# Kernel optimization log

Hardware: AMD Instinct MI355X
Metric: run time of the kernel (lower is better)

## Reference

```python
import jax, jax.numpy as jnp
import numpy as np
from jax import lax

# Model / data dims (match init_kwargs / input_specs)
B, SEQ_LEN, IN_DIM, HID, TGT, PRED_LEN = 64, 1024, 128, 256, 128, 192
NUM_SCALES, TOP_K, KS = 2, 3, 3
DN = ('NCHW', 'OIHW', 'NCHW')


def avg_pool1d(x):
    # stride-2 average pool over last axis: [B,C,T] -> [B,C,T//2]
    b, c, t = x.shape
    return x[..., : (t // 2) * 2].reshape(b, c, t // 2, 2).mean(-1)


def dsconv2d(z, dw_w, dw_b, pw_w, pw_b):
    # depthwise 3x3 (groups=C_in, SAME pad) + pointwise 1x1 (C_in -> HID)
    c = z.shape[1]
    y = lax.conv_general_dilated(z, dw_w, (1, 1), 'SAME',
                                 feature_group_count=c, dimension_numbers=DN)
    y = y + dw_b[None, :, None, None]
    y = lax.conv_general_dilated(y, pw_w, (1, 1), 'SAME', dimension_numbers=DN)
    return y + pw_b[None, :, None, None]


def mean_amplitudes(xm):
    # xm: [B,C,T]; mean |rfft| over batch and channels, DC component zeroed
    a = jnp.abs(jnp.fft.rfft(xm, axis=-1)).mean(axis=(0, 1))
    return a.at[0].set(0.0)


def topk_freqs(xm, k):
    # concrete (eager) top-k frequency indices -> python ints (mirrors .item())
    amps = mean_amplitudes(xm)
    idx = np.asarray(lax.top_k(amps, k)[1])
    return [max(1, int(i)) for i in idx]


def setup_inputs() -> dict:
    key = jax.random.key(0)
    ks = jax.random.split(key, 8)
    s = 0.05
    return {
        'x': jax.random.normal(ks[0], (B, SEQ_LEN, IN_DIM), jnp.float32),
        'dw_w': jax.random.normal(ks[1], (IN_DIM, 1, KS, KS), jnp.float32) * s,
        'dw_b': jnp.zeros((IN_DIM,), jnp.float32),
        'pw_w': jax.random.normal(ks[2], (HID, IN_DIM, 1, 1), jnp.float32) * s,
        'pw_b': jnp.zeros((HID,), jnp.float32),
        'w_t0': jax.random.normal(ks[3], (PRED_LEN, SEQ_LEN), jnp.float32) * s,
        'b_t0': jnp.zeros((PRED_LEN,), jnp.float32),
        'w_t1': jax.random.normal(ks[4], (PRED_LEN, SEQ_LEN // 2), jnp.float32) * s,
        'b_t1': jnp.zeros((PRED_LEN,), jnp.float32),
        'w_t2': jax.random.normal(ks[5], (PRED_LEN, SEQ_LEN // 4), jnp.float32) * s,
        'b_t2': jnp.zeros((PRED_LEN,), jnp.float32),
        'w_ch': jax.random.normal(ks[6], (TGT, HID), jnp.float32) * s,
        'b_ch': jnp.zeros((TGT,), jnp.float32),
        'scale_logits': jnp.zeros((NUM_SCALES + 1,), jnp.float32),
    }


def _forward(x, dw_w, dw_b, pw_w, pw_b, time_ws, time_bs, w_ch, b_ch,
             scale_logits, freqs_per_scale):
    x_ct = jnp.transpose(x, (0, 2, 1))  # [B,C,T]
    scales = [x_ct]
    for _ in range(NUM_SCALES):
        scales.append(avg_pool1d(scales[-1]))
    sw = jax.nn.softmax(scale_logits) * float(NUM_SCALES + 1)
    y_sum = 0.0
    for m, xm in enumerate(scales):
        t = xm.shape[-1]
        amps = mean_amplitudes(xm)
        freqs = freqs_per_scale[m]
        wk = jax.nn.softmax(amps[jnp.array(freqs)])  # softmax over top-k amps
        fused = 0.0
        for k, f in enumerate(freqs):
            p = t // f                      # period (python int)
            rows = -(-t // p)               # ceil(t / p)
            pad = rows * p - t
            z = jnp.pad(xm, ((0, 0), (0, 0), (0, pad)))
            z = z.reshape(xm.shape[0], xm.shape[1], rows, p)  # 1D -> 2D grid
            y2 = dsconv2d(z, dw_w, dw_b, pw_w, pw_b)          # [B,HID,rows,p]
            y1 = y2.reshape(y2.shape[0], HID, rows * p)[..., :t]
            fused = fused + wk[k] * y1
        # dropout is identity in eval mode; l_m == time_projs[m].in_features here
        pred = jnp.einsum('bhl,pl->bph', fused, time_ws[m]) + time_bs[m][None, :, None]
        y_m = jnp.einsum('bph,oh->bpo', pred, w_ch) + b_ch
        y_sum = y_sum + sw[m] * y_m
    # residual: seq_len >= pred_len, input_dim == target_dim -> plain slice add
    return y_sum + x[:, -PRED_LEN:, :]


def reference(x, dw_w, dw_b, pw_w, pw_b, w_t0, b_t0, w_t1, b_t1, w_t2, b_t2,
              w_ch, b_ch, scale_logits):
    scales = [jnp.transpose(x, (0, 2, 1))]
    for _ in range(NUM_SCALES):
        scales.append(avg_pool1d(scales[-1]))
    freqs_per_scale = [topk_freqs(xm, TOP_K) for xm in scales]
    return _forward(x, dw_w, dw_b, pw_w, pw_b, [w_t0, w_t1, w_t2],
                    [b_t0, b_t1, b_t2], w_ch, b_ch, scale_logits, freqs_per_scale)
```

## Files before the change

### kernel.cpp

```cpp
#include <hip/hip_runtime.h>
#include <math.h>

#define NB   64
#define T0   1024
#define CIN  128
#define HID  256
#define TGT  128
#define PRED 192
#define NROWS (NB*CIN)
#define KTOT 1792

typedef __attribute__((ext_vector_type(4))) float f32x4;
typedef __attribute__((ext_vector_type(8))) short s16x8;

static const size_t XCT_OFF    = 0;
static const size_t S1_OFF     = 8388608;
static const size_t S2_OFF     = 12582912;
static const size_t P0_OFF     = 14680064;
static const size_t PARTS2_OFF = 15622144;
static const size_t META_OFF   = 15647104;
static const size_t W2T_OFF    = 15647168;
static const size_t PBS_OFF    = 15655360;
static const size_t WSUM_OFF   = 15655616;
static const size_t TB32_OFF   = 15656192;
static const size_t TB16_OFF   = 15659264;
static const size_t WTB_OFF    = 15660800;
static const size_t DWM_OFF    = 15832832;
static const size_t TP_OFF     = 23172864;

__device__ inline unsigned short f2bf(float x) {
    union { float f; unsigned u; } v; v.f = x;
    unsigned r = (v.u + 0x7FFFu + ((v.u >> 16) & 1u)) >> 16;
    return (unsigned short)r;
}
__device__ inline float bf2f(unsigned short u) {
    union { unsigned u; float f; } v; v.u = ((unsigned)u) << 16;
    return v.f;
}

__global__ __launch_bounds__(256) void front(const float* __restrict__ x,
        float* __restrict__ xct, float* __restrict__ s1, float* __restrict__ s2) {
    __shared__ float tile[32][33];
    int b = blockIdx.z;
    int t0 = blockIdx.x * 32, c0 = blockIdx.y * 32;
    int tx = threadIdx.x, ty = threadIdx.y;
#pragma unroll
    for (int i = 0; i < 4; i++) {
        int t = t0 + ty + i * 8, c = c0 + tx;
        tile[ty + i * 8][tx] = x[((size_t)b * T0 + t) * CIN + c];
    }
    __syncthreads();
#pragma unroll
    for (int i = 0; i < 4; i++) {
        int c = c0 + ty + i * 8, cc = ty + i * 8;
        xct[((size_t)b * CIN + c) * T0 + t0 + tx] = tile[tx][cc];
        if (tx < 16) {
            float v = 0.5f * (tile[2 * tx][cc] + tile[2 * tx + 1][cc]);
            s1[((size_t)b * CIN + c) * (T0 / 2) + t0 / 2 + tx] = v;
        }
        if (tx < 8) {
            float v = 0.25f * (tile[4 * tx][cc] + tile[4 * tx + 1][cc]
                             + tile[4 * tx + 2][cc] + tile[4 * tx + 3][cc]);
            s2[((size_t)b * CIN + c) * (T0 / 4) + t0 / 4 + tx] = v;
        }
    }
}

#define PHYS(i) ((i) + ((i) >> 5))
template<int LOGT>
__device__ __forceinline__ void fft_body(const float* __restrict__ xm,
        float* __restrict__ part, int pad,
        float* re, float* im, float* twc, float* tws, float* acc) {
    constexpr int T = 1 << LOGT;
    constexpr int F = T / 2;
    int tid = threadIdx.x;
    for (int j = tid; j < F; j += 256) {
        float s, c;
        sincosf(-6.283185307179586f * (float)j / (float)T, &s, &c);
        twc[PHYS(j)] = c; tws[PHYS(j)] = s;
    }
    for (int i = tid; i <= F; i += 256) acc[i] = 0.f;
    __syncthreads();

    int rowbase = blockIdx.x * 8;
    for (int pr = 0; pr < 4; pr++) {
        const float* row0 = xm + (size_t)(rowbase + 2 * pr) * T;
        const float* row1 = row0 + T;
        for (int j = tid; j < T; j += 256) {
            int rv = (int)(__brev((unsigned)j) >> (32 - LOGT));
            re[PHYS(rv)] = row0[j];
            im[PHYS(rv)] = row1[j];
        }
        __syncthreads();
        for (int s = 1; s + 1 <= LOGT; s += 2) {
            int mh = 1 << (s - 1);
            if (tid < T / 4) {
                int k  = tid & (mh - 1);
                int gq = tid >> (s - 1);
                int i0 = (gq << (s + 1)) + k;
                int iA = PHYS(i0), iB = PHYS(i0 + mh);
                int iC = PHYS(i0 + 2 * mh), iD = PHYS(i0 + 3 * mh);
                int t1 = PHYS(k << (LOGT - s));
                int t2 = PHYS(k << (LOGT - s - 1));
                int t3 = PHYS((k + mh) << (LOGT - s - 1));
                float w1r = twc[t1], w1i = tws[t1];
                float w2r = twc[t2], w2i = tws[t2];
                float w3r = twc[t3], w3i = tws[t3];
                float ar = re[iA], ai = im[iA];
                float br = re[iB], bi = im[iB];
                float cr = re[iC], ci = im[iC];
                float dr = re[iD], di = im[iD];
                float tbr = w1r * br - w1i * bi, tbi = w1r * bi + w1i * br;
                float tdr = w1r * dr - w1i * di, tdi = w1r * di + w1i * dr;
                float v0r = ar + tbr, v0i = ai + tbi;
                float v1r = ar - tbr, v1i = ai - tbi;
                float v2r = cr + tdr, v2i = ci + tdi;
                float v3r = cr - tdr, v3i = ci - tdi;
                float t2r = w2r * v2r - w2i * v2i, t2i = w2r * v2i + w2i * v2r;
                float t3r = w3r * v3r - w3i * v3i, t3i = w3r * v3i + w3i * v3r;
                re[iA] = v0r + t2r; im[iA] = v0i + t2i;
                re[iC] = v0r - t2r; im[iC] = v0i - t2i;
                re[iB] = v1r + t3r; im[iB] = v1i + t3i;
                re[iD] = v1r - t3r; im[iD] = v1i - t3i;
            }
            __syncthreads();
        }
        if (LOGT & 1) {
            constexpr int s = LOGT;
            int mh = 1 << (s - 1);
            if (tid < T / 2) {
                int k  = tid & (mh - 1);
                int i1 = PHYS(tid);
                int i2 = PHYS(tid + mh);
                int tw = PHYS(k);
                float wr = twc[tw], wi = tws[tw];
                float xr = re[i2], xi = im[i2];
                float tr = wr * xr - wi * xi;
                float ti = wr * xi + wi * xr;
                float ur = re[i1], ui = im[i1];
                re[i1] = ur + tr; im[i1] = ui + ti;
                re[i2] = ur - tr; im[i2] = ui - ti;
            }
            __syncthreads();
        }
        for (int f = tid; f <= F; f += 256) {
            if (f >= 1) {
                int mf = T - f;
                float rf = re[PHYS(f)], imf = im[PHYS(f)];
                float rm = re[PHYS(mf)], imm = im[PHYS(mf)];
                float m0 = sqrtf((rf + rm) * (rf + rm) + (imf - imm) * (imf - imm));
                float m1 = sqrtf((imf + imm) * (imf + imm) + (rf - rm) * (rf - rm));
                acc[f] += 0.5f * (m0 + m1);
            }
        }
        __syncthreads();
    }
    for (int f = tid; f <= F; f += 256)
        part[(size_t)blockIdx.x * pad + f] = acc[f];
}

__global__ __launch_bounds__(256) void fft_all(const float* __restrict__ xct,
        const float* __restrict__ s1, const float* __restrict__ s2,
        float* __restrict__ parts) {
    __shared__ float re[1056], im[1056], twc[528], tws[528], acc[513];
    int sc = blockIdx.y;
    if (sc == 0)
        fft_body<10>(xct, parts, 520, re, im, twc, tws, acc);
    else if (sc == 1)
        fft_body<9>(s1, parts + (size_t)1024 * 520, 264, re, im, twc, tws, acc);
    else
        fft_body<8>(s2, parts + (size_t)1024 * 520 + (size_t)1024 * 264, 136,
                    re, im, twc, tws, acc);
}

__global__ __launch_bounds__(256) void reduce_partA(const float* __restrict__ parts,
                                                    float* __restrict__ parts2) {
    const int PADs[3] = {520, 264, 136};
    const int Fs[3]   = {513, 257, 129};
    const size_t POFF[3] = {0, (size_t)1024 * 520, (size_t)1024 * 520 + (size_t)1024 * 264};
    int s  = blockIdx.y;
    int rs = blockIdx.z;
    int fl = threadIdx.x & 63;
    int rg = threadIdx.x >> 6;
    int f  = blockIdx.x * 64 + fl;
    bool valid = f < Fs[s];
    const float* base = parts + POFF[s];
    int pad = PADs[s];
    float sum = 0.f;
    if (valid) {
        int r0 = rs * 64 + rg * 16;
#pragma unroll
        for (int i = 0; i < 16; i++) sum += base[(size_t)(r0 + i) * pad + f];
    }
    __shared__ float red[256];
    red[threadIdx.x] = sum;
    __syncthreads();
    if (rg == 0 && valid) {
        float tot = red[fl] + red[fl + 64] + red[fl + 128] + red[fl + 192];
        parts2[(size_t)(s * 16 + rs) * 520 + f] = tot;
    }
}

__device__ inline float sum16(const float* __restrict__ p2, int m, int f) {
    const float* b = p2 + (size_t)m * 16 * 520 + f;
    float s = 0.f;
#pragma unroll
    for (int r = 0; r < 16; r++) s += b[r * 520];
    return s;
}

__device__ inline void ins3(float v, int i, float& b0, int& c0,
                            float& b1, int& c1, float& b2, int& c2) {
    bool g0 = (v > b0) || (v == b0 && i < c0);
    bool g1 = (v > b1) || (v == b1 && i < c1);
    bool g2 = (v > b2) || (v == b2 && i < c2);
    if (g0)      { b2 = b1; c2 = c1; b1 = b0; c1 = c0; b0 = v; c0 = i; }
    else if (g1) { b2 = b1; c2 = c1; b1 = v; c1 = i; }
    else if (g2) { b2 = v; c2 = i; }
}

__global__ __launch_bounds__(256) void meta_topk(const float* __restrict__ parts2,
                          const float* __restrict__ slog,
                          int* __restrict__ freqs, float* __restrict__ wk,
                          float* __restrict__ sw,
                          unsigned* __restrict__ tb32g, unsigned short* __restrict__ tb16g) {
    __shared__ float sv[12];
    __shared__ int   si[12];
    __shared__ int   sfr[3];
    const int Fs[3] = {513, 257, 129};
    const int Ts[3] = {1024, 512, 256};
    int m = blockIdx.x;
    int tid = threadIdx.x, lane = tid & 63, wv = tid >> 6;
    int F = Fs[m];
    float b0 = -1e30f, b1 = -1e30f, b2 = -1e30f;
    int   c0 = 0x7fffffff, c1 = 0x7fffffff, c2 = 0x7fffffff;
    for (int i = tid; i < F; i += 256) {
        float v = (i == 0) ? 0.f : sum16(parts2, m, i) * (1.f / 8192.f);
        ins3(v, i, b0, c0, b1, c1, b2, c2);
    }
#pragma unroll
    for (int d = 1; d < 64; d <<= 1) {
        float o0 = __shfl_xor(b0, d), o1 = __shfl_xor(b1, d), o2 = __shfl_xor(b2, d);
        int   i0 = __shfl_xor(c0, d), i1 = __shfl_xor(c1, d), i2 = __shfl_xor(c2, d);
        ins3(o0, i0, b0, c0, b1, c1, b2, c2);
        ins3(o1, i1, b0, c0, b1, c1, b2, c2);
        ins3(o2, i2, b0, c0, b1, c1, b2, c2);
    }
    if (lane == 0) {
        sv[wv * 3 + 0] = b0; si[wv * 3 + 0] = c0;
        sv[wv * 3 + 1] = b1; si[wv * 3 + 1] = c1;
        sv[wv * 3 + 2] = b2; si[wv * 3 + 2] = c2;
    }
    __syncthreads();
    if (tid == 0) {
        float d0 = sv[0], d1 = sv[1], d2 = sv[2];
        int   e0 = si[0], e1 = si[1], e2 = si[2];
        for (int q = 3; q < 12; q++) ins3(sv[q], si[q], d0, e0, d1, e1, d2, e2);
        int fr[3] = {max(1, e0), max(1, e1), max(1, e2)};
        float av[3];
#pragma unroll
        for (int i = 0; i < 3; i++) av[i] = sum16(parts2, m, fr[i]) * (1.f / 8192.f);
        float mx = fmaxf(av[0], fmaxf(av[1], av[2]));
        float x0 = expf(av[0] - mx), x1 = expf(av[1] - mx), x2 = expf(av[2] - mx);
        float inv = 1.f / (x0 + x1 + x2);
        freqs[m * 3 + 0] = fr[0]; freqs[m * 3 + 1] = fr[1]; freqs[m * 3 + 2] = fr[2];
        wk[m * 3 + 0] = x0 * inv; wk[m * 3 + 1] = x1 * inv; wk[m * 3 + 2] = x2 * inv;
        sfr[0] = fr[0]; sfr[1] = fr[1]; sfr[2] = fr[2];
        if (m == 0) {
            float s0 = slog[0], s1 = slog[1], s2 = slog[2];
            float mx2 = fmaxf(s0, fmaxf(s1, s2));
            float e0b = expf(s0 - mx2), e1b = expf(s1 - mx2), e2b = expf(s2 - mx2);
            float inv2 = 3.f / (e0b + e1b + e2b);
            sw[0] = e0b * inv2; sw[1] = e1b * inv2; sw[2] = e2b * inv2;
        }
    }
    __syncthreads();
    int Tm = Ts[m];
    int p0 = Tm / sfr[0], p1 = Tm / sfr[1], p2v = Tm / sfr[2];
    int S0 = (p0 + 2) | 1, S1 = (p1 + 2) | 1, S2v = (p2v + 2) | 1;
    int r0n = (Tm + p0 - 1) / p0, r1n = (Tm + p1 - 1) / p1;
    int off0 = 0;
    int off1 = (r0n + 2) * S0;
    int off2 = off1 + (r1n + 2) * S1;
    for (int l = tid; l < Tm; l += 256) {
        int ra = l / p0, ca = l - ra * p0;
        int rb = l / p1, cb = l - rb * p1;
        int rc = l / p2v, cc = l - rc * p2v;
        unsigned ba = off0 + (ra + 1) * S0 + ca + 1;
        unsigned bb = off1 + (rb + 1) * S1 + cb + 1;
        unsigned bc = off2 + (rc + 1) * S2v + cc + 1;
        tb32g[m * 1024 + l] = ba | (bb << 16);
        tb16g[m * 1024 + l] = (unsigned short)bc;
    }
}

__global__ __launch_bounds__(256) void prep_all(const float* __restrict__ w_ch,
        const float* __restrict__ pw_w, const float* __restrict__ pw_b,
        const float* __restrict__ wt0, const float* __restrict__ wt1,
        const float* __restrict__ wt2, const float* __restrict__ swb,
        unsigned short* __restrict__ w2ot, float* __restrict__ pbs,
        unsigned short* __restrict__ wtb, float* __restrict__ wsum) {
    int tid = threadIdx.x;
    int bx = blockIdx.x;
    if (bx < 64) {
        int idx = bx * 256 + tid;
        int c = idx >> 7, o = idx & 127;
        float acc = 0.f;
        for (int h = 0; h < HID; h++) acc += w_ch[o * HID + h] * pw_w[h * CIN + c];
        w2ot[o * 128 + (c ^ ((o & 7) << 3))] = f2bf(acc);
        return;
    }
    if (bx == 64) {
        if (tid < 128) {
            float pb = 0.f, s = 0.f;
            for (int h = 0; h < HID; h++) {
                float w = w_ch[tid * HID + h];
                pb += w * pw_b[h]; s += w;
            }
            pbs[tid] = pb; pbs[128 + tid] = s;
        }
        return;
    }
    int wid = (bx - 65) * 4 + (tid >> 6);
    int lane = tid & 63;
    const float* src; int T, p, m; int moff;
    if (wid < 192)      { m = 0; p = wid;       src = wt0; T = 1024; moff = 0; }
    else if (wid < 384) { m = 1; p = wid - 192; src = wt1; T = 512;  moff = 1024; }
    else                { m = 2; p = wid - 384; src = wt2; T = 256;  moff = 1536; }
    float swm = swb[m];
    const float* row = src + (size_t)p * T;
    unsigned short* dst = wtb + (size_t)p * KTOT + moff;
    float s = 0.f;
    for (int j = lane; j < T; j += 64) {
        float v = row[j] * swm; s += v; dst[j] = f2bf(v);
    }
#pragma unroll
    for (int d = 1; d < 64; d <<= 1) s += __shfl_xor(s, d);
    if (lane == 0) wsum[m * 192 + p] = s;
}

template<int T>
__device__ __forceinline__ void dwmix_body(const float* __restrict__ xm,
        const float* __restrict__ dw_w, const float* __restrict__ dw_b,
        const int* __restrict__ freqs, const float* __restrict__ wkbuf,
        const unsigned* __restrict__ tb32g, const unsigned short* __restrict__ tb16g,
        int m, int moff, unsigned short* __restrict__ dwm, float* xs) {
    constexpr int NP = T / 256;
    int tid = threadIdx.x;
    int c = blockIdx.x, b = blockIdx.y;
    int S0, S1, S2; float wkv[3]; int tot;
    {
        int off = 0; int Sv[3];
#pragma unroll
        for (int k = 0; k < 3; k++) {
            int f = freqs[m * 3 + k];
            int p = T / f;
            int S = (p + 2) | 1;
            Sv[k] = S;
            int rows = (T + p - 1) / p;
            off += (rows + 2) * S;
            wkv[k] = wkbuf[m * 3 + k];
        }
        S0 = Sv[0]; S1 = Sv[1]; S2 = Sv[2]; tot = off;
    }
    for (int i = tid; i < tot; i += 256) xs[i] = 0.f;
    __syncthreads();
    const float* src = xm + ((size_t)b * CIN + c) * T;
    const unsigned* t32 = tb32g + m * 1024;
    const unsigned short* t16 = tb16g + m * 1024;
    unsigned w32r[NP]; int b2r[NP];
#pragma unroll
    for (int i = 0; i < NP; i++) {
        int l = i * 256 + tid;
        float xv = src[l];
        unsigned w32 = t32[l];
        int b2v = t16[l];
        w32r[i] = w32; b2r[i] = b2v;
        xs[w32 & 0xffff] = xv;
        xs[w32 >> 16]    = xv;
        xs[b2v]          = xv;
    }
    __syncthreads();

    float wk9[27];
#pragma unroll
    for (int k = 0; k < 3; k++)
#pragma unroll
        for (int q = 0; q < 9; q++) wk9[k * 9 + q] = wkv[k] * dw_w[c * 9 + q];
    float bias = dw_b[c];
    unsigned short* outp = dwm + (size_t)(b * CIN + c) * KTOT + moff;

#pragma unroll
    for (int i = 0; i < NP; i++) {
        unsigned w32 = w32r[i];
        const float* q0 = xs + (w32 & 0xffff);
        const float* q1 = xs + (w32 >> 16);
        const float* q2 = xs + b2r[i];
        float a0 = wk9[0] * q0[-S0 - 1] + wk9[1] * q0[-S0] + wk9[2] * q0[-S0 + 1]
                 + wk9[3] * q0[-1]      + wk9[4] * q0[0]   + wk9[5] * q0[1]
                 + wk9[6] * q0[S0 - 1]  + wk9[7] * q0[S0]  + wk9[8] * q0[S0 + 1];
        float a1 = wk9[9]  * q1[-S1 - 1] + wk9[10] * q1[-S1] + wk9[11] * q1[-S1 + 1]
                 + wk9[12] * q1[-1]      + wk9[13] * q1[0]   + wk9[14] * q1[1]
                 + wk9[15] * q1[S1 - 1]  + wk9[16] * q1[S1]  + wk9[17] * q1[S1 + 1];
        float a2 = wk9[18] * q2[-S2 - 1] + wk9[19] * q2[-S2] + wk9[20] * q2[-S2 + 1]
                 + wk9[21] * q2[-1]      + wk9[22] * q2[0]   + wk9[23] * q2[1]
                 + wk9[24] * q2[S2 - 1]  + wk9[25] * q2[S2]  + wk9[26] * q2[S2 + 1];
        outp[i * 256 + tid] = f2bf(bias + a0 + a1 + a2);
    }
}

__global__ __launch_bounds__(256) void dwmix_all(const float* __restrict__ xct,
        const float* __restrict__ s1, const float* __restrict__ s2,
        const float* __restrict__ dw_w, const float* __restrict__ dw_b,
        const int* __restrict__ freqs, const float* __restrict__ wkbuf,
        const unsigned* __restrict__ tb32g, const unsigned short* __restrict__ tb16g,
        unsigned short* __restrict__ dwm) {
    __shared__ float xs[7232];
    int sc = blockIdx.z;
    if (sc == 0)
        dwmix_body<1024>(xct, dw_w, dw_b, freqs, wkbuf, tb32g, tb16g, 0, 0, dwm, xs);
    else if (sc == 1)
        dwmix_body<512>(s1, dw_w, dw_b, freqs, wkbuf, tb32g, tb16g, 1, 1024, dwm, xs);
    else
        dwmix_body<256>(s2, dw_w, dw_b, freqs, wkbuf, tb32g, tb16g, 2, 1536, dwm, xs);
}

__global__ __launch_bounds__(256) void tp_gemm(const unsigned short* __restrict__ A,
        const unsigned short* __restrict__ B, unsigned short* __restrict__ C) {
    __shared__ __align__(16) unsigned short As[64 * 72];
    __shared__ __align__(16) unsigned short Bs[64 * 72];
    int tid = threadIdx.x;
    int lane = tid & 63, wave = tid >> 6;
    int wm = (wave >> 1) * 32, wn = (wave & 1) * 32;
    int p0 = blockIdx.x * 64, n0 = blockIdx.y * 64;
    f32x4 acc[2][2];
#pragma unroll
    for (int i = 0; i < 2; i++)
#pragma unroll
        for (int j = 0; j < 2; j++) acc[i][j] = (f32x4){0.f, 0.f, 0.f, 0.f};

    int r = tid >> 2, seg = tid & 3;
    const unsigned short* ga = A + (size_t)(p0 + r) * KTOT + seg * 16;
    const unsigned short* gb = B + (size_t)(n0 + r) * KTOT + seg * 16;
    unsigned short* la = &As[r * 72 + seg * 16];
    unsigned short* lb = &Bs[r * 72 + seg * 16];
    int fr = lane & 15, fk = (lane >> 4) * 8;

    for (int k0 = 0; k0 < KTOT; k0 += 64) {
        __syncthreads();
        *(uint4*)la       = *(const uint4*)ga;
        *(uint4*)(la + 8) = *(const uint4*)(ga + 8);
        *(uint4*)lb       = *(const uint4*)gb;
        *(uint4*)(lb + 8) = *(const uint4*)(gb + 8);
        ga += 64; gb += 64;
        __syncthreads();
#pragma unroll
        for (int ks = 0; ks < 2; ks++) {
            int ko = ks * 32 + fk;
            s16x8 a0 = *(const s16x8*)&As[(wm + fr) * 72 + ko];
            s16x8 a1 = *(const s16x8*)&As[(wm + 16 + fr) * 72 + ko];
            s16x8 b0 = *(const s16x8*)&Bs[(wn + fr) * 72 + ko];
            s16x8 b1 = *(const s16x8*)&Bs[(wn + 16 + fr) * 72 + ko];
            acc[0][0] = __builtin_amdgcn_mfma_f32_16x16x32_bf16(a0, b0, acc[0][0], 0, 0, 0);
            acc[0][1] = __builtin_amdgcn_mfma_f32_16x16x32_bf16(a0, b1, acc[0][1], 0, 0, 0);
            acc[1][0] = __builtin_amdgcn_mfma_f32_16x16x32_bf16(a1, b0, acc[1][0], 0, 0, 0);
            acc[1][1] = __builtin_amdgcn_mfma_f32_16x16x32_bf16(a1, b1, acc[1][1], 0, 0, 0);
        }
    }
    int crow = (lane >> 4) * 4, ccol = lane & 15;
#pragma unroll
    for (int i = 0; i < 2; i++)
#pragma unroll
        for (int j = 0; j < 2; j++) {
            int col = n0 + wn + j * 16 + ccol;
#pragma unroll
            for (int reg = 0; reg < 4; reg++) {
                int row = p0 + wm + i * 16 + crow + reg;
                C[(size_t)row * 8192 + col] = f2bf(acc[i][j][reg]);
            }
        }
}

__global__ __launch_bounds__(256) void final_out(const float* __restrict__ x,
        const unsigned short* __restrict__ tp, const unsigned short* __restrict__ w2ot,
        const float* __restrict__ pbs, const float* __restrict__ wsum,
        const float* __restrict__ bt0, const float* __restrict__ bt1,
        const float* __restrict__ bt2, const float* __restrict__ b_ch,
        const float* __restrict__ swb, float* __restrict__ out) {
    __shared__ unsigned short w2s[128 * 128];
    __shared__ float tpsS[32][128];
    __shared__ float wsS[32], btS[32];
    int tid = threadIdx.x;
    int r0 = blockIdx.x * 32;
    float sw0 = swb[0], sw1 = swb[1], sw2 = swb[2];

#pragma unroll
    for (int i = 0; i < 8; i++)
        ((uint4*)w2s)[i * 256 + tid] = ((const uint4*)w2ot)[i * 256 + tid];
#pragma unroll
    for (int it = 0; it < 2; it++) {
        int idx = tid + it * 256;
        int rr = idx >> 4, u = idx & 15;
        int r = r0 + rr;
        int b2 = r / 192, p2 = r - b2 * 192;
        size_t base = (size_t)p2 * 8192 + (size_t)b2 * 128 + u * 8;
        uint4 q0 = *(const uint4*)&tp[base];
        const unsigned* a0 = (const unsigned*)&q0;
        float o8[8];
#pragma unroll
        for (int w = 0; w < 4; w++) {
            o8[2 * w]     = bf2f(a0[w] & 0xffff);
            o8[2 * w + 1] = bf2f(a0[w] >> 16);
        }
        *(float4*)&tpsS[rr][u * 8]     = *(float4*)&o8[0];
        *(float4*)&tpsS[rr][u * 8 + 4] = *(float4*)&o8[4];
    }
    if (tid < 32) {
        int r = r0 + tid;
        int b2 = r / 192, p = r - b2 * 192;
        wsS[tid] = wsum[p] + wsum[192 + p] + wsum[384 + p];
        btS[tid] = sw0 * bt0[p] + sw1 * bt1[p] + sw2 * bt2[p];
    }
    __syncthreads();

    int o = tid & 127, half = tid >> 7;
    int rbase = half * 16;
    float pbv  = pbs[o];
    float schv = pbs[128 + o];
    float bchv = (sw0 + sw1 + sw2) * b_ch[o];
    float acc[16];
#pragma unroll
    for (int rr = 0; rr < 16; rr++) acc[rr] = 0.f;

#pragma unroll 2
    for (int cb8 = 0; cb8 < 16; cb8++) {
        uint4 wv = *(const uint4*)&w2s[o * 128 + ((cb8 ^ (o & 7)) << 3)];
        const unsigned* aw = (const unsigned*)&wv;
        float wf[8];
#pragma unroll
        for (int w = 0; w < 4; w++) {
            wf[2 * w]     = bf2f(aw[w] & 0xffff);
            wf[2 * w + 1] = bf2f(aw[w] >> 16);
        }
        int cc = cb8 * 8;
#pragma unroll
        for (int rr = 0; rr < 16; rr++) {
            const float* tr = &tpsS[rbase + rr][cc];
            float4 t0 = *(const float4*)tr;
            float4 t1 = *(const float4*)(tr + 4);
            acc[rr] += wf[0] * t0.x + wf[1] * t0.y + wf[2] * t0.z + wf[3] * t0.w
                     + wf[4] * t1.x + wf[5] * t1.y + wf[6] * t1.z + wf[7] * t1.w;
        }
    }
#pragma unroll
    for (int rr = 0; rr < 16; rr++) {
        int r = r0 + rbase + rr;
        int b2 = r / 192, p = r - b2 * 192;
        float res = x[((size_t)b2 * T0 + (T0 - PRED) + p) * CIN + o];
        out[(size_t)r * TGT + o] = res + acc[rr] + pbv * wsS[rbase + rr]
                                 + schv * btS[rbase + rr] + bchv;
    }
}

extern "C" void kernel_launch(void* const* d_in, const int* in_sizes, int n_in,
                              void* d_out, int out_size, void* d_ws, size_t ws_size,
                              hipStream_t stream) {
    const float* x    = (const float*)d_in[0];
    const float* dw_w = (const float*)d_in[1];
    const float* dw_b = (const float*)d_in[2];
    const float* pw_w = (const float*)d_in[3];
    const float* pw_b = (const float*)d_in[4];
    const float* wt0  = (const float*)d_in[5];
    const float* bt0  = (const float*)d_in[6];
    const float* wt1  = (const float*)d_in[7];
    const float* bt1  = (const float*)d_in[8];
    const float* wt2  = (const float*)d_in[9];
    const float* bt2  = (const float*)d_in[10];
    const float* w_ch = (const float*)d_in[11];
    const float* b_ch = (const float*)d_in[12];
    const float* slog = (const float*)d_in[13];
    float* out = (float*)d_out;
    float* ws  = (float*)d_ws;

    float* xct    = ws + XCT_OFF;
    float* s1b    = ws + S1_OFF;
    float* s2b    = ws + S2_OFF;
    float* parts  = ws + P0_OFF;
    float* parts2 = ws + PARTS2_OFF;
    int*   freqs  = (int*)(ws + META_OFF);
    float* wkb    = ws + META_OFF + 16;
    float* swb    = ws + META_OFF + 32;
    unsigned short* w2tb = (unsigned short*)(ws + W2T_OFF);
    float* pbs    = ws + PBS_OFF;
    float* wsumb  = ws + WSUM_OFF;
    unsigned*       tb32g = (unsigned*)(ws + TB32_OFF);
    unsigned short* tb16g = (unsigned short*)(ws + TB16_OFF);
    unsigned short* wtb  = (unsigned short*)(ws + WTB_OFF);
    unsigned short* dwm  = (unsigned short*)(ws + DWM_OFF);
    unsigned short* tpb  = (unsigned short*)(ws + TP_OFF);

    front<<<dim3(32, 4, NB), dim3(32, 8, 1), 0, stream>>>(x, xct, s1b, s2b);
    fft_all<<<dim3(1024, 3), 256, 0, stream>>>(xct, s1b, s2b, parts);
    reduce_partA<<<dim3(9, 3, 16), 256, 0, stream>>>(parts, parts2);
    meta_topk<<<3, 256, 0, stream>>>(parts2, slog, freqs, wkb, swb, tb32g, tb16g);
    prep_all<<<209, 256, 0, stream>>>(w_ch, pw_w, pw_b, wt0, wt1, wt2, swb,
                                      w2tb, pbs, wtb, wsumb);
    dwmix_all<<<dim3(CIN, NB, 3), 256, 0, stream>>>(xct, s1b, s2b, dw_w, dw_b,
                                                    freqs, wkb, tb32g, tb16g, dwm);
    tp_gemm<<<dim3(3, 128), 256, 0, stream>>>(wtb, dwm, tpb);
    final_out<<<384, 256, 0, stream>>>(x, tpb, w2tb, pbs, wsumb,
                                       bt0, bt1, bt2, b_ch, swb, out);
}
```

Before: 198.7 us.

## Fuse weight prep into FFT launch, merge first radix-4 stage into load, split dwmix

Folds the weight-preparation kernel into the FFT launch as an extra grid slice, recomputing the softmax scale weights locally from the logits so it no longer depends on meta_topk. The FFT now does the first radix-4 butterfly while loading the bit-reversed inputs, which removes one shared-memory pass and sync per row pair. The depthwise mix kernel is split so the smaller scales use a smaller shared buffer, which can raise occupancy. The cost is more register pressure in the fused FFT kernel and one extra kernel launch for dwmix.

```diff
diff --git a/kernel.cpp b/kernel.cpp
--- a/kernel.cpp
+++ b/kernel.cpp
@@ -66,6 +66,58 @@
     }
 }
 
+__device__ void prep_body(const float* __restrict__ w_ch,
+        const float* __restrict__ pw_w, const float* __restrict__ pw_b,
+        const float* __restrict__ wt0, const float* __restrict__ wt1,
+        const float* __restrict__ wt2, const float* __restrict__ slog,
+        unsigned short* __restrict__ w2ot, float* __restrict__ pbs,
+        unsigned short* __restrict__ wtb, float* __restrict__ wsum) {
+    int tid = threadIdx.x;
+    int bx = blockIdx.x;
+    if (bx >= 209) return;
+    if (bx < 64) {
+        int idx = bx * 256 + tid;
+        int c = idx >> 7, o = idx & 127;
+        float acc = 0.f;
+        for (int h = 0; h < HID; h++) acc += w_ch[o * HID + h] * pw_w[h * CIN + c];
+        w2ot[o * 128 + (c ^ ((o & 7) << 3))] = f2bf(acc);
+        return;
+    }
+    if (bx == 64) {
+        if (tid < 128) {
+            float pb = 0.f, s = 0.f;
+            for (int h = 0; h < HID; h++) {
+                float w = w_ch[tid * HID + h];
+                pb += w * pw_b[h]; s += w;
+            }
+            pbs[tid] = pb; pbs[128 + tid] = s;
+        }
+        return;
+    }
+    float s0l = slog[0], s1l = slog[1], s2l = slog[2];
+    float mx = fmaxf(s0l, fmaxf(s1l, s2l));
+    float e0 = expf(s0l - mx), e1 = expf(s1l - mx), e2 = expf(s2l - mx);
+    float inv = 3.f / (e0 + e1 + e2);
+    float swl[3] = {e0 * inv, e1 * inv, e2 * inv};
+
+    int wid = (bx - 65) * 4 + (tid >> 6);
+    int lane = tid & 63;
+    const float* src; int T, p, m; int moff;
+    if (wid < 192)      { m = 0; p = wid;       src = wt0; T = 1024; moff = 0; }
+    else if (wid < 384) { m = 1; p = wid - 192; src = wt1; T = 512;  moff = 1024; }
+    else                { m = 2; p = wid - 384; src = wt2; T = 256;  moff = 1536; }
+    float swm = swl[m];
+    const float* row = src + (size_t)p * T;
+    unsigned short* dst = wtb + (size_t)p * KTOT + moff;
+    float s = 0.f;
+    for (int j = lane; j < T; j += 64) {
+        float v = row[j] * swm; s += v; dst[j] = f2bf(v);
+    }
+#pragma unroll
+    for (int d = 1; d < 64; d <<= 1) s += __shfl_xor(s, d);
+    if (lane == 0) wsum[m * 192 + p] = s;
+}
+
 #define PHYS(i) ((i) + ((i) >> 5))
 template<int LOGT>
 __device__ __forceinline__ void fft_body(const float* __restrict__ xm,
@@ -86,13 +138,24 @@
     for (int pr = 0; pr < 4; pr++) {
         const float* row0 = xm + (size_t)(rowbase + 2 * pr) * T;
         const float* row1 = row0 + T;
-        for (int j = tid; j < T; j += 256) {
-            int rv = (int)(__brev((unsigned)j) >> (32 - LOGT));
-            re[PHYS(rv)] = row0[j];
-            im[PHYS(rv)] = row1[j];
+        if (tid < T / 4) {
+            int base = (LOGT > 2) ? (int)(__brev((unsigned)tid) >> (32 - (LOGT - 2))) : 0;
+            float x0r = row0[base],             x0i = row1[base];
+            float x1r = row0[base + T / 2],     x1i = row1[base + T / 2];
+            float x2r = row0[base + T / 4],     x2i = row1[base + T / 4];
+            float x3r = row0[base + 3 * T / 4], x3i = row1[base + 3 * T / 4];
+            float ar = x0r + x1r, ai = x0i + x1i;
+            float br = x0r - x1r, bi = x0i - x1i;
+            float cr = x2r + x3r, ci = x2i + x3i;
+            float dr = x2r - x3r, di = x2i - x3i;
+            int o = 4 * tid;
+            re[PHYS(o)]     = ar + cr;  im[PHYS(o)]     = ai + ci;
+            re[PHYS(o + 2)] = ar - cr;  im[PHYS(o + 2)] = ai - ci;
+            re[PHYS(o + 1)] = br + di;  im[PHYS(o + 1)] = bi - dr;
+            re[PHYS(o + 3)] = br - di;  im[PHYS(o + 3)] = bi + dr;
         }
         __syncthreads();
-        for (int s = 1; s + 1 <= LOGT; s += 2) {
+        for (int s = 3; s + 1 <= LOGT; s += 2) {
             int mh = 1 << (s - 1);
             if (tid < T / 4) {
                 int k  = tid & (mh - 1);
@@ -161,9 +224,19 @@
 
 __global__ __launch_bounds__(256) void fft_all(const float* __restrict__ xct,
         const float* __restrict__ s1, const float* __restrict__ s2,
-        float* __restrict__ parts) {
+        float* __restrict__ parts,
+        const float* __restrict__ w_ch, const float* __restrict__ pw_w,
+        const float* __restrict__ pw_b, const float* __restrict__ wt0,
+        const float* __restrict__ wt1, const float* __restrict__ wt2,
+        const float* __restrict__ slog,
+        unsigned short* __restrict__ w2ot, float* __restrict__ pbs,
+        unsigned short* __restrict__ wtb, float* __restrict__ wsum) {
     __shared__ float re[1056], im[1056], twc[528], tws[528], acc[513];
     int sc = blockIdx.y;
+    if (sc == 3) {
+        prep_body(w_ch, pw_w, pw_b, wt0, wt1, wt2, slog, w2ot, pbs, wtb, wsum);
+        return;
+    }
     if (sc == 0)
         fft_body<10>(xct, parts, 520, re, im, twc, tws, acc);
     else if (sc == 1)
@@ -294,51 +367,6 @@
     }
 }
 
-__global__ __launch_bounds__(256) void prep_all(const float* __restrict__ w_ch,
-        const float* __restrict__ pw_w, const float* __restrict__ pw_b,
-        const float* __restrict__ wt0, const float* __restrict__ wt1,
-        const float* __restrict__ wt2, const float* __restrict__ swb,
-        unsigned short* __restrict__ w2ot, float* __restrict__ pbs,
-        unsigned short* __restrict__ wtb, float* __restrict__ wsum) {
-    int tid = threadIdx.x;
-    int bx = blockIdx.x;
-    if (bx < 64) {
-        int idx = bx * 256 + tid;
-        int c = idx >> 7, o = idx & 127;
-        float acc = 0.f;
-        for (int h = 0; h < HID; h++) acc += w_ch[o * HID + h] * pw_w[h * CIN + c];
-        w2ot[o * 128 + (c ^ ((o & 7) << 3))] = f2bf(acc);
-        return;
-    }
-    if (bx == 64) {
-        if (tid < 128) {
-            float pb = 0.f, s = 0.f;
-            for (int h = 0; h < HID; h++) {
-                float w = w_ch[tid * HID + h];
-                pb += w * pw_b[h]; s += w;
-            }
-            pbs[tid] = pb; pbs[128 + tid] = s;
-        }
-        return;
-    }
-    int wid = (bx - 65) * 4 + (tid >> 6);
-    int lane = tid & 63;
-    const float* src; int T, p, m; int moff;
-    if (wid < 192)      { m = 0; p = wid;       src = wt0; T = 1024; moff = 0; }
-    else if (wid < 384) { m = 1; p = wid - 192; src = wt1; T = 512;  moff = 1024; }
-    else                { m = 2; p = wid - 384; src = wt2; T = 256;  moff = 1536; }
-    float swm = swb[m];
-    const float* row = src + (size_t)p * T;
-    unsigned short* dst = wtb + (size_t)p * KTOT + moff;
-    float s = 0.f;
-    for (int j = lane; j < T; j += 64) {
-        float v = row[j] * swm; s += v; dst[j] = f2bf(v);
-    }
-#pragma unroll
-    for (int d = 1; d < 64; d <<= 1) s += __shfl_xor(s, d);
-    if (lane == 0) wsum[m * 192 + p] = s;
-}
-
 template<int T>
 __device__ __forceinline__ void dwmix_body(const float* __restrict__ xm,
         const float* __restrict__ dw_w, const float* __restrict__ dw_b,
@@ -409,17 +437,23 @@
     }
 }
 
-__global__ __launch_bounds__(256) void dwmix_all(const float* __restrict__ xct,
-        const float* __restrict__ s1, const float* __restrict__ s2,
+__global__ __launch_bounds__(256) void dwmix_s0(const float* __restrict__ xct,
         const float* __restrict__ dw_w, const float* __restrict__ dw_b,
         const int* __restrict__ freqs, const float* __restrict__ wkbuf,
         const unsigned* __restrict__ tb32g, const unsigned short* __restrict__ tb16g,
         unsigned short* __restrict__ dwm) {
     __shared__ float xs[7232];
-    int sc = blockIdx.z;
-    if (sc == 0)
-        dwmix_body<1024>(xct, dw_w, dw_b, freqs, wkbuf, tb32g, tb16g, 0, 0, dwm, xs);
-    else if (sc == 1)
+    dwmix_body<1024>(xct, dw_w, dw_b, freqs, wkbuf, tb32g, tb16g, 0, 0, dwm, xs);
+}
+
+__global__ __launch_bounds__(256) void dwmix_s12(const float* __restrict__ s1,
+        const float* __restrict__ s2,
+        const float* __restrict__ dw_w, const float* __restrict__ dw_b,
+        const int* __restrict__ freqs, const float* __restrict__ wkbuf,
+        const unsigned* __restrict__ tb32g, const unsigned short* __restrict__ tb16g,
+        unsigned short* __restrict__ dwm) {
+    __shared__ float xs[3648];
+    if (blockIdx.z == 0)
         dwmix_body<512>(s1, dw_w, dw_b, freqs, wkbuf, tb32g, tb16g, 1, 1024, dwm, xs);
     else
         dwmix_body<256>(s2, dw_w, dw_b, freqs, wkbuf, tb32g, tb16g, 2, 1536, dwm, xs);
@@ -600,13 +634,15 @@
     unsigned short* tpb  = (unsigned short*)(ws + TP_OFF);
 
     front<<<dim3(32, 4, NB), dim3(32, 8, 1), 0, stream>>>(x, xct, s1b, s2b);
-    fft_all<<<dim3(1024, 3), 256, 0, stream>>>(xct, s1b, s2b, parts);
+    fft_all<<<dim3(1024, 4), 256, 0, stream>>>(xct, s1b, s2b, parts,
+                                               w_ch, pw_w, pw_b, wt0, wt1, wt2, slog,
+                                               w2tb, pbs, wtb, wsumb);
     reduce_partA<<<dim3(9, 3, 16), 256, 0, stream>>>(parts, parts2);
     meta_topk<<<3, 256, 0, stream>>>(parts2, slog, freqs, wkb, swb, tb32g, tb16g);
-    prep_all<<<209, 256, 0, stream>>>(w_ch, pw_w, pw_b, wt0, wt1, wt2, swb,
-                                      w2tb, pbs, wtb, wsumb);
-    dwmix_all<<<dim3(CIN, NB, 3), 256, 0, stream>>>(xct, s1b, s2b, dw_w, dw_b,
-                                                    freqs, wkb, tb32g, tb16g, dwm);
+    dwmix_s0<<<dim3(CIN, NB), 256, 0, stream>>>(xct, dw_w, dw_b, freqs, wkb,
+                                                tb32g, tb16g, dwm);
+    dwmix_s12<<<dim3(CIN, NB, 2), 256, 0, stream>>>(s1b, s2b, dw_w, dw_b, freqs, wkb,
+                                                    tb32g, tb16g, dwm);
     tp_gemm<<<dim3(3, 128), 256, 0, stream>>>(wtb, dwm, tpb);
     final_out<<<384, 256, 0, stream>>>(x, tpb, w2tb, pbs, wsumb,
                                        bt0, bt1, bt2, b_ch, swb, out);
```

Result: faster. 194.6 us (median of 2 runs) (-2.0%).
